# Optimization experiments

Measured on AMD Instinct MI355X. Metric: run time of the kernel, lower is better.

Reference implementation:

```python
import jax, jax.numpy as jnp
import numpy as np

COMMITMENT_COST = 0.25


def setup_inputs() -> dict:
    key = jax.random.key(0)
    k1, k2 = jax.random.split(key)
    inputs = jax.random.normal(k1, (16, 4096, 256), dtype=jnp.float32)
    codewords = jax.random.normal(k2, (1024, 256), dtype=jnp.float32)
    return {"inputs": inputs, "codewords": codewords}


def reference(inputs, codewords):
    # inputs: (*, D), codewords: (K, D)
    D = codewords.shape[-1]
    flat = inputs.reshape(-1, D)  # (N, D)
    x_sq = jnp.sum(flat * flat, axis=-1, keepdims=True)            # (N, 1)
    c_sq = jnp.sum(codewords * codewords, axis=-1)                 # (K,)
    distances = x_sq - 2.0 * (flat @ codewords.T) + c_sq           # (N, K)
    encoding_indices = jnp.argmin(distances, axis=1)               # (N,)
    quantized = codewords[encoding_indices].reshape(inputs.shape)  # (*, D)
    # Straight-through estimator
    quantized_st = inputs + jax.lax.stop_gradient(quantized - inputs)
    quantizing_loss = jnp.mean((quantized_st - jax.lax.stop_gradient(inputs)) ** 2)
    commitment_loss = jnp.mean((jax.lax.stop_gradient(quantized_st) - inputs) ** 2)
    loss = quantizing_loss + COMMITMENT_COST * commitment_loss
    return quantized_st, encoding_indices.reshape(inputs.shape[:-1]), loss
```

## Files before the change

kernel.cpp:

```cpp
#include <hip/hip_runtime.h>
#include <math.h>

typedef _Float16 v8h __attribute__((ext_vector_type(8)));
typedef float v4f __attribute__((ext_vector_type(4)));

constexpr int D      = 256;
constexpr int NTILE  = 64;
constexpr int KS     = 8;
constexpr int TILE_B = 8192;
constexpr int WIN_B  = 16384;
#define GUARD 2.0f

__global__ void vq_prep(const float* __restrict__ cw, unsigned short* __restrict__ img) {
    int gid = blockIdx.x * 256 + threadIdx.x;
    int t  = gid >> 9;
    int r  = gid & 511;
    int ks = r >> 6;
    int l  = r & 63;
    int cand = t * 16 + (l & 15);
    int k0   = ks * 32 + (l >> 4) * 8;
    const float* src = cw + (size_t)cand * D + k0;
    float4 t0 = *(const float4*)(src);
    float4 t1 = *(const float4*)(src + 4);
    v8h h;
    h[0] = (_Float16)t0.x; h[1] = (_Float16)t0.y;
    h[2] = (_Float16)t0.z; h[3] = (_Float16)t0.w;
    h[4] = (_Float16)t1.x; h[5] = (_Float16)t1.y;
    h[6] = (_Float16)t1.z; h[7] = (_Float16)t1.w;
    *(v8h*)((char*)img + (size_t)gid * 16) = h;
}

__global__ void vq_csq(const float* __restrict__ cw, float* __restrict__ csq) {
    int k = blockIdx.x * blockDim.x + threadIdx.x;
    const float4* p = reinterpret_cast<const float4*>(cw + (size_t)k * D);
    float s = 0.f;
    #pragma unroll 8
    for (int i = 0; i < D / 4; ++i) {
        float4 v = p[i];
        s += v.x * v.x; s += v.y * v.y; s += v.z * v.z; s += v.w * v.w;
    }
    csq[k] = s;
}

__launch_bounds__(256, 2)
__global__ void vq_mfma(const float* __restrict__ inp,
                        const unsigned short* __restrict__ img,
                        const float* __restrict__ csq,
                        int* __restrict__ pack,
                        float* __restrict__ xsqbuf) {
    __shared__ char smem[2][WIN_B];

    const int tid  = threadIdx.x;
    const int lane = tid & 63;
    const int w    = tid >> 6;
    const int lr   = lane & 15;
    const int q    = lane >> 4;
    const int base = blockIdx.x * 128 + w * 32;

    #pragma unroll
    for (int i = 0; i < 4; ++i) {
        int off = i * 4096 + w * 1024;
        __builtin_amdgcn_global_load_lds(
            (const __attribute__((address_space(1))) unsigned int*)((const char*)img + off + lane * 16),
            (__attribute__((address_space(3))) unsigned int*)(&smem[0][off]),
            16, 0, 0);
    }

    v8h a2[2][8];
    #pragma unroll
    for (int m = 0; m < 2; ++m) {
        const float* rp = inp + (size_t)(base + m * 16 + lr) * D + q * 8;
        float sq = 0.f;
        #pragma unroll
        for (int ks = 0; ks < KS; ++ks) {
            float4 t0 = *(const float4*)(rp + ks * 32);
            float4 t1 = *(const float4*)(rp + ks * 32 + 4);
            sq = fmaf(t0.x, t0.x, sq); sq = fmaf(t0.y, t0.y, sq);
            sq = fmaf(t0.z, t0.z, sq); sq = fmaf(t0.w, t0.w, sq);
            sq = fmaf(t1.x, t1.x, sq); sq = fmaf(t1.y, t1.y, sq);
            sq = fmaf(t1.z, t1.z, sq); sq = fmaf(t1.w, t1.w, sq);
            v8h h;
            h[0] = (_Float16)(-2.f * t0.x); h[1] = (_Float16)(-2.f * t0.y);
            h[2] = (_Float16)(-2.f * t0.z); h[3] = (_Float16)(-2.f * t0.w);
            h[4] = (_Float16)(-2.f * t1.x); h[5] = (_Float16)(-2.f * t1.y);
            h[6] = (_Float16)(-2.f * t1.z); h[7] = (_Float16)(-2.f * t1.w);
            a2[m][ks] = h;
        }
        sq += __shfl_xor(sq, 16);
        sq += __shfl_xor(sq, 32);
        if (q == 0) xsqbuf[base + m * 16 + lr] = sq;
    }

    const float BIGF = __uint_as_float(0x7F000000u);
    float v1[2][4], v2[2][4];
    #pragma unroll
    for (int m = 0; m < 2; ++m)
        #pragma unroll
        for (int r = 0; r < 4; ++r) { v1[m][r] = BIGF; v2[m][r] = BIGF; }

    asm volatile("s_waitcnt vmcnt(0)" ::: "memory");
    __builtin_amdgcn_s_barrier();
    __builtin_amdgcn_sched_barrier(0);

    int cur = 0;
    for (int win = 0; win < NTILE / 2; ++win) {
        if (win + 1 < NTILE / 2) {
            const char* srct = (const char*)img + (size_t)(win + 1) * WIN_B;
            #pragma unroll
            for (int i = 0; i < 4; ++i) {
                int off = i * 4096 + w * 1024;
                __builtin_amdgcn_global_load_lds(
                    (const __attribute__((address_space(1))) unsigned int*)(srct + off + lane * 16),
                    (__attribute__((address_space(3))) unsigned int*)(&smem[cur ^ 1][off]),
                    16, 0, 0);
            }
        }
        float cqA = csq[(2 * win) * 16 + lr] + 4096.f;
        float cqB = csq[(2 * win + 1) * 16 + lr] + 4096.f;

        const char* bb = smem[cur];
        v4f aA0 = {cqA, cqA, cqA, cqA}; v4f aA1 = aA0;
        v4f aB0 = {cqB, cqB, cqB, cqB}; v4f aB1 = aB0;
        #pragma unroll
        for (int ks = 0; ks < KS; ++ks) {
            v8h bA = *(const v8h*)(bb + ks * 1024 + lane * 16);
            v8h bB = *(const v8h*)(bb + TILE_B + ks * 1024 + lane * 16);
            aA0 = __builtin_amdgcn_mfma_f32_16x16x32_f16(a2[0][ks], bA, aA0, 0, 0, 0);
            aB0 = __builtin_amdgcn_mfma_f32_16x16x32_f16(a2[0][ks], bB, aB0, 0, 0, 0);
            aA1 = __builtin_amdgcn_mfma_f32_16x16x32_f16(a2[1][ks], bA, aA1, 0, 0, 0);
            aB1 = __builtin_amdgcn_mfma_f32_16x16x32_f16(a2[1][ks], bB, aB1, 0, 0, 0);
        }
        unsigned idxA = (unsigned)((2 * win) * 16) | (unsigned)lr;
        unsigned idxB = (unsigned)((2 * win + 1) * 16) | (unsigned)lr;
        #pragma unroll
        for (int r = 0; r < 4; ++r) {
            float f;
            f = __uint_as_float(((__float_as_uint(aA0[r]) + 0x200u) & 0xFFFFFC00u) | idxA);
            { float mx = fmaxf(v1[0][r], f); v2[0][r] = fminf(v2[0][r], mx); v1[0][r] = fminf(v1[0][r], f); }
            f = __uint_as_float(((__float_as_uint(aA1[r]) + 0x200u) & 0xFFFFFC00u) | idxA);
            { float mx = fmaxf(v1[1][r], f); v2[1][r] = fminf(v2[1][r], mx); v1[1][r] = fminf(v1[1][r], f); }
            f = __uint_as_float(((__float_as_uint(aB0[r]) + 0x200u) & 0xFFFFFC00u) | idxB);
            { float mx = fmaxf(v1[0][r], f); v2[0][r] = fminf(v2[0][r], mx); v1[0][r] = fminf(v1[0][r], f); }
            f = __uint_as_float(((__float_as_uint(aB1[r]) + 0x200u) & 0xFFFFFC00u) | idxB);
            { float mx = fmaxf(v1[1][r], f); v2[1][r] = fminf(v2[1][r], mx); v1[1][r] = fminf(v1[1][r], f); }
        }

        asm volatile("s_waitcnt vmcnt(0)" ::: "memory");
        __builtin_amdgcn_s_barrier();
        __builtin_amdgcn_sched_barrier(0);
        cur ^= 1;
    }

    #pragma unroll
    for (int m = 0; m < 2; ++m)
        #pragma unroll
        for (int r = 0; r < 4; ++r) {
            float L0 = v1[m][r], L1 = v2[m][r], L2 = BIGF, L3 = BIGF;
            #pragma unroll
            for (int off = 8; off; off >>= 1) {
                float P0 = __shfl_xor(L0, off, 16);
                float P1 = __shfl_xor(L1, off, 16);
                float P2 = __shfl_xor(L2, off, 16);
                float P3 = __shfl_xor(L3, off, 16);
                float M0 = fminf(L0, P3), M1 = fminf(L1, P2);
                float M2 = fminf(L2, P1), M3 = fminf(L3, P0);
                float a0 = fminf(M0, M2), c0 = fmaxf(M0, M2);
                float b0 = fminf(M1, M3), d0 = fmaxf(M1, M3);
                L0 = fminf(a0, b0); L1 = fmaxf(a0, b0);
                L2 = fminf(c0, d0); L3 = fmaxf(c0, d0);
            }
            if (lr == 0) {
                int row = base + m * 16 + q * 4 + r;
                ((int4*)pack)[row] = make_int4(
                    (int)__float_as_uint(L0), (int)__float_as_uint(L1),
                    (int)__float_as_uint(L2), (int)__float_as_uint(L3));
            }
        }
}

__launch_bounds__(256)
__global__ void vq_out(const float* __restrict__ inp,
                       const float* __restrict__ cw,
                       const float* __restrict__ csq,
                       const int* __restrict__ pack,
                       const float* __restrict__ xsqbuf,
                       float* __restrict__ outq,
                       float* __restrict__ outi,
                       float* __restrict__ bsum) {
    __shared__ float s_l[4];
    const int tid  = threadIdx.x;
    const int lane = tid & 63;
    const int wv   = tid >> 6;
    const int g    = blockIdx.x * 256 + tid;
    const int row  = g >> 2;
    const int c    = g & 3;

    int4 pk = ((const int4*)pack)[row];
    float s0 = __uint_as_float((unsigned)pk.x);
    float s1 = __uint_as_float((unsigned)pk.y);
    float xq = xsqbuf[row];

    int   bi;
    float bd;
    bool rescue = (s1 - s0) < GUARD;
    if (rescue) {
        int cd = ((c == 0) ? pk.x : (c == 1) ? pk.y : (c == 2) ? pk.z : pk.w) & 1023;
        const float4* xp = (const float4*)(inp + (size_t)row * D);
        const float4* cp = (const float4*)(cw + (size_t)cd * D);
        float dot = 0.f, xsq = 0.f;
        #pragma unroll 8
        for (int i = 0; i < D / 4; ++i) {
            float4 xv = xp[i];
            float4 cv = cp[i];
            xsq = fmaf(xv.x, xv.x, xsq);
            xsq = fmaf(xv.y, xv.y, xsq);
            xsq = fmaf(xv.z, xv.z, xsq);
            xsq = fmaf(xv.w, xv.w, xsq);
            dot = fmaf(xv.x, cv.x, dot);
            dot = fmaf(xv.y, cv.y, dot);
            dot = fmaf(xv.z, cv.z, dot);
            dot = fmaf(xv.w, cv.w, dot);
        }
        float m2 = dot + dot;
        float t  = xsq - m2;
        float e  = t + csq[cd];
        bd = e; bi = cd;
        #pragma unroll
        for (int off = 1; off <= 2; off <<= 1) {
            float ev = __shfl_xor(bd, off, 4);
            int   iv = __shfl_xor(bi, off, 4);
            bool  tk = (ev < bd) || (ev == bd && iv < bi);
            bd = tk ? ev : bd;
            bi = tk ? iv : bi;
        }
    } else {
        bi = pk.x & 1023;
        bd = (s0 - 4096.f) + xq;
    }

    if (c == 0) outi[row] = (float)bi;

    float lc = (c == 0) ? bd : 0.f;
    #pragma unroll
    for (int off = 32; off; off >>= 1) lc += __shfl_xor(lc, off);
    if (lane == 0) s_l[wv] = lc;
    __syncthreads();
    if (tid == 0) bsum[blockIdx.x] = s_l[0] + s_l[1] + s_l[2] + s_l[3];

    const int rowbase = blockIdx.x * 64 + wv * 16;
    #pragma unroll 4
    for (int rr = 0; rr < 16; ++rr) {
        int bw = __shfl(bi, rr * 4, 64);
        float4 cv = *(const float4*)(cw + (size_t)bw * D + lane * 4);
        *(float4*)(outq + (size_t)(rowbase + rr) * D + lane * 4) = cv;
    }
}

__global__ void vq_finalize(const float* __restrict__ bsum, float* __restrict__ out_loss,
                            int nb, float scale) {
    __shared__ float s[4];
    int tid = threadIdx.x;
    float v = 0.f;
    for (int i = tid; i < nb; i += 256) v += bsum[i];
    #pragma unroll
    for (int off = 32; off; off >>= 1) v += __shfl_down(v, off, 64);
    if ((tid & 63) == 0) s[tid >> 6] = v;
    __syncthreads();
    if (tid == 0) out_loss[0] = (s[0] + s[1] + s[2] + s[3]) * scale;
}

extern "C" void kernel_launch(void* const* d_in, const int* in_sizes, int n_in,
                              void* d_out, int out_size, void* d_ws, size_t ws_size,
                              hipStream_t stream) {
    const float* inp = (const float*)d_in[0];
    const float* cw  = (const float*)d_in[1];
    float* out = (float*)d_out;
    const int N = in_sizes[0] / D;
    const int K = in_sizes[1] / D;

    char* ws = (char*)d_ws;
    unsigned short* img = (unsigned short*)ws;
    float* csq    = (float*)(ws + (size_t)K * D * 2);
    float* bsum   = csq + K;
    int*   pack   = (int*)(bsum + 1024);
    float* xsqbuf = (float*)(pack + (size_t)N * 4);

    float* outq = out;
    float* outi = out + (size_t)N * D;
    float* outl = outi + N;

    vq_prep<<<dim3((K * 32) / 256), dim3(256), 0, stream>>>(cw, img);
    vq_csq<<<dim3(K / 256), dim3(256), 0, stream>>>(cw, csq);

    vq_mfma<<<dim3(N / 128), dim3(256), 0, stream>>>(inp, img, csq, pack, xsqbuf);
    vq_out<<<dim3(N / 64), dim3(256), 0, stream>>>(inp, cw, csq, pack, xsqbuf,
                                                   outq, outi, bsum);
    vq_finalize<<<dim3(1), dim3(256), 0, stream>>>(bsum, outl, N / 64,
                                                   1.25f / ((float)N * (float)D));
}
```

Measured before the change: 99.54 us.

## Split codebook search across two grid halves and merge top-4 lists in output kernel

```diff
diff --git a/kernel.cpp b/kernel.cpp
--- a/kernel.cpp
+++ b/kernel.cpp
@@ -9,6 +9,7 @@
 constexpr int KS     = 8;
 constexpr int TILE_B = 8192;
 constexpr int WIN_B  = 16384;
+constexpr int HWIN   = 16;
 #define GUARD 2.0f
 
 __global__ void vq_prep(const float* __restrict__ cw, unsigned short* __restrict__ img) {
@@ -42,7 +43,7 @@
     csq[k] = s;
 }
 
-__launch_bounds__(256, 2)
+__launch_bounds__(256, 4)
 __global__ void vq_mfma(const float* __restrict__ inp,
                         const unsigned short* __restrict__ img,
                         const float* __restrict__ csq,
@@ -55,13 +56,15 @@
     const int w    = tid >> 6;
     const int lr   = lane & 15;
     const int q    = lane >> 4;
+    const int hh   = blockIdx.y;
     const int base = blockIdx.x * 128 + w * 32;
+    const char* imgh = (const char*)img + (size_t)hh * 32 * TILE_B;
 
     #pragma unroll
     for (int i = 0; i < 4; ++i) {
         int off = i * 4096 + w * 1024;
         __builtin_amdgcn_global_load_lds(
-            (const __attribute__((address_space(1))) unsigned int*)((const char*)img + off + lane * 16),
+            (const __attribute__((address_space(1))) unsigned int*)(imgh + off + lane * 16),
             (__attribute__((address_space(3))) unsigned int*)(&smem[0][off]),
             16, 0, 0);
     }
@@ -88,7 +91,7 @@
         }
         sq += __shfl_xor(sq, 16);
         sq += __shfl_xor(sq, 32);
-        if (q == 0) xsqbuf[base + m * 16 + lr] = sq;
+        if (hh == 0 && q == 0) xsqbuf[base + m * 16 + lr] = sq;
     }
 
     const float BIGF = __uint_as_float(0x7F000000u);
@@ -103,9 +106,9 @@
     __builtin_amdgcn_sched_barrier(0);
 
     int cur = 0;
-    for (int win = 0; win < NTILE / 2; ++win) {
-        if (win + 1 < NTILE / 2) {
-            const char* srct = (const char*)img + (size_t)(win + 1) * WIN_B;
+    for (int win = 0; win < HWIN; ++win) {
+        if (win + 1 < HWIN) {
+            const char* srct = imgh + (size_t)(win + 1) * WIN_B;
             #pragma unroll
             for (int i = 0; i < 4; ++i) {
                 int off = i * 4096 + w * 1024;
@@ -115,8 +118,10 @@
                     16, 0, 0);
             }
         }
-        float cqA = csq[(2 * win) * 16 + lr] + 4096.f;
-        float cqB = csq[(2 * win + 1) * 16 + lr] + 4096.f;
+        const int tA = hh * 32 + 2 * win;
+        const int tB = tA + 1;
+        float cqA = csq[tA * 16 + lr] + 4096.f;
+        float cqB = csq[tB * 16 + lr] + 4096.f;
 
         const char* bb = smem[cur];
         v4f aA0 = {cqA, cqA, cqA, cqA}; v4f aA1 = aA0;
@@ -130,8 +135,8 @@
             aA1 = __builtin_amdgcn_mfma_f32_16x16x32_f16(a2[1][ks], bA, aA1, 0, 0, 0);
             aB1 = __builtin_amdgcn_mfma_f32_16x16x32_f16(a2[1][ks], bB, aB1, 0, 0, 0);
         }
-        unsigned idxA = (unsigned)((2 * win) * 16) | (unsigned)lr;
-        unsigned idxB = (unsigned)((2 * win + 1) * 16) | (unsigned)lr;
+        unsigned idxA = (unsigned)(tA * 16) | (unsigned)lr;
+        unsigned idxB = (unsigned)(tB * 16) | (unsigned)lr;
         #pragma unroll
         for (int r = 0; r < 4; ++r) {
             float f;
@@ -171,7 +176,7 @@
             }
             if (lr == 0) {
                 int row = base + m * 16 + q * 4 + r;
-                ((int4*)pack)[row] = make_int4(
+                ((int4*)pack)[(size_t)row * 2 + hh] = make_int4(
                     (int)__float_as_uint(L0), (int)__float_as_uint(L1),
                     (int)__float_as_uint(L2), (int)__float_as_uint(L3));
             }
@@ -195,16 +200,26 @@
     const int row  = g >> 2;
     const int c    = g & 3;
 
-    int4 pk = ((const int4*)pack)[row];
-    float s0 = __uint_as_float((unsigned)pk.x);
-    float s1 = __uint_as_float((unsigned)pk.y);
+    int4 pa = ((const int4*)pack)[(size_t)row * 2 + 0];
+    int4 pb = ((const int4*)pack)[(size_t)row * 2 + 1];
+    float a0 = __uint_as_float((unsigned)pa.x), a1 = __uint_as_float((unsigned)pa.y);
+    float a2 = __uint_as_float((unsigned)pa.z), a3 = __uint_as_float((unsigned)pa.w);
+    float b0 = __uint_as_float((unsigned)pb.x), b1 = __uint_as_float((unsigned)pb.y);
+    float b2 = __uint_as_float((unsigned)pb.z), b3 = __uint_as_float((unsigned)pb.w);
+    float M0 = fminf(a0, b3), M1 = fminf(a1, b2), M2 = fminf(a2, b1), M3 = fminf(a3, b0);
+    float t0 = fminf(M0, M2), t2 = fmaxf(M0, M2);
+    float t1 = fminf(M1, M3), t3 = fmaxf(M1, M3);
+    float L0 = fminf(t0, t1), L1 = fmaxf(t0, t1);
+    float L2 = fminf(t2, t3), L3 = fmaxf(t2, t3);
+
     float xq = xsqbuf[row];
 
     int   bi;
     float bd;
-    bool rescue = (s1 - s0) < GUARD;
+    bool rescue = (L1 - L0) < GUARD;
     if (rescue) {
-        int cd = ((c == 0) ? pk.x : (c == 1) ? pk.y : (c == 2) ? pk.z : pk.w) & 1023;
+        float Lc = (c == 0) ? L0 : (c == 1) ? L1 : (c == 2) ? L2 : L3;
+        int cd = (int)(__float_as_uint(Lc) & 1023u);
         const float4* xp = (const float4*)(inp + (size_t)row * D);
         const float4* cp = (const float4*)(cw + (size_t)cd * D);
         float dot = 0.f, xsq = 0.f;
@@ -234,8 +249,8 @@
             bi = tk ? iv : bi;
         }
     } else {
-        bi = pk.x & 1023;
-        bd = (s0 - 4096.f) + xq;
+        bi = (int)(__float_as_uint(L0) & 1023u);
+        bd = (L0 - 4096.f) + xq;
     }
 
     if (c == 0) outi[row] = (float)bi;
@@ -283,7 +298,7 @@
     float* csq    = (float*)(ws + (size_t)K * D * 2);
     float* bsum   = csq + K;
     int*   pack   = (int*)(bsum + 1024);
-    float* xsqbuf = (float*)(pack + (size_t)N * 4);
+    float* xsqbuf = (float*)(pack + (size_t)N * 8);
 
     float* outq = out;
     float* outi = out + (size_t)N * D;
@@ -292,7 +307,7 @@
     vq_prep<<<dim3((K * 32) / 256), dim3(256), 0, stream>>>(cw, img);
     vq_csq<<<dim3(K / 256), dim3(256), 0, stream>>>(cw, csq);
 
-    vq_mfma<<<dim3(N / 128), dim3(256), 0, stream>>>(inp, img, csq, pack, xsqbuf);
+    vq_mfma<<<dim3(N / 128, 2), dim3(256), 0, stream>>>(inp, img, csq, pack, xsqbuf);
     vq_out<<<dim3(N / 64), dim3(256), 0, stream>>>(inp, cw, csq, pack, xsqbuf,
                                                    outq, outi, bsum);
     vq_finalize<<<dim3(1), dim3(256), 0, stream>>>(bsum, outl, N / 64,
```

New measurement: 111.1 us. +11.6%, slower.

## Fuse rescue/output stage into MFMA kernel via shared-memory handoff

Applied to the files above, without the earlier changes.

```diff
diff --git a/kernel.cpp b/kernel.cpp
--- a/kernel.cpp
+++ b/kernel.cpp
@@ -43,12 +43,18 @@
 }
 
 __launch_bounds__(256, 2)
-__global__ void vq_mfma(const float* __restrict__ inp,
+__global__ void vq_main(const float* __restrict__ inp,
+                        const float* __restrict__ cw,
                         const unsigned short* __restrict__ img,
                         const float* __restrict__ csq,
-                        int* __restrict__ pack,
-                        float* __restrict__ xsqbuf) {
-    __shared__ char smem[2][WIN_B];
+                        float* __restrict__ outq,
+                        float* __restrict__ outi,
+                        float* __restrict__ bsum) {
+    __shared__ char  smem[2][WIN_B];
+    __shared__ int4  s_pack[128];
+    __shared__ float s_xsq[128];
+    __shared__ int   s_win[128];
+    __shared__ float s_l[4];
 
     const int tid  = threadIdx.x;
     const int lane = tid & 63;
@@ -88,7 +94,7 @@
         }
         sq += __shfl_xor(sq, 16);
         sq += __shfl_xor(sq, 32);
-        if (q == 0) xsqbuf[base + m * 16 + lr] = sq;
+        if (q == 0) s_xsq[w * 32 + m * 16 + lr] = sq;
     }
 
     const float BIGF = __uint_as_float(0x7F000000u);
@@ -170,90 +176,81 @@
                 L2 = fminf(c0, d0); L3 = fmaxf(c0, d0);
             }
             if (lr == 0) {
-                int row = base + m * 16 + q * 4 + r;
-                ((int4*)pack)[row] = make_int4(
+                int rloc = m * 16 + q * 4 + r;
+                s_pack[w * 32 + rloc] = make_int4(
                     (int)__float_as_uint(L0), (int)__float_as_uint(L1),
                     (int)__float_as_uint(L2), (int)__float_as_uint(L3));
             }
         }
-}
-
-__launch_bounds__(256)
-__global__ void vq_out(const float* __restrict__ inp,
-                       const float* __restrict__ cw,
-                       const float* __restrict__ csq,
-                       const int* __restrict__ pack,
-                       const float* __restrict__ xsqbuf,
-                       float* __restrict__ outq,
-                       float* __restrict__ outi,
-                       float* __restrict__ bsum) {
-    __shared__ float s_l[4];
-    const int tid  = threadIdx.x;
-    const int lane = tid & 63;
-    const int wv   = tid >> 6;
-    const int g    = blockIdx.x * 256 + tid;
-    const int row  = g >> 2;
-    const int c    = g & 3;
-
-    int4 pk = ((const int4*)pack)[row];
-    float s0 = __uint_as_float((unsigned)pk.x);
-    float s1 = __uint_as_float((unsigned)pk.y);
-    float xq = xsqbuf[row];
-
-    int   bi;
-    float bd;
-    bool rescue = (s1 - s0) < GUARD;
-    if (rescue) {
-        int cd = ((c == 0) ? pk.x : (c == 1) ? pk.y : (c == 2) ? pk.z : pk.w) & 1023;
-        const float4* xp = (const float4*)(inp + (size_t)row * D);
-        const float4* cp = (const float4*)(cw + (size_t)cd * D);
-        float dot = 0.f, xsq = 0.f;
-        #pragma unroll 8
-        for (int i = 0; i < D / 4; ++i) {
-            float4 xv = xp[i];
-            float4 cv = cp[i];
-            xsq = fmaf(xv.x, xv.x, xsq);
-            xsq = fmaf(xv.y, xv.y, xsq);
-            xsq = fmaf(xv.z, xv.z, xsq);
-            xsq = fmaf(xv.w, xv.w, xsq);
-            dot = fmaf(xv.x, cv.x, dot);
-            dot = fmaf(xv.y, cv.y, dot);
-            dot = fmaf(xv.z, cv.z, dot);
-            dot = fmaf(xv.w, cv.w, dot);
-        }
-        float m2 = dot + dot;
-        float t  = xsq - m2;
-        float e  = t + csq[cd];
-        bd = e; bi = cd;
-        #pragma unroll
-        for (int off = 1; off <= 2; off <<= 1) {
-            float ev = __shfl_xor(bd, off, 4);
-            int   iv = __shfl_xor(bi, off, 4);
-            bool  tk = (ev < bd) || (ev == bd && iv < bi);
-            bd = tk ? ev : bd;
-            bi = tk ? iv : bi;
-        }
-    } else {
-        bi = pk.x & 1023;
-        bd = (s0 - 4096.f) + xq;
-    }
-
-    if (c == 0) outi[row] = (float)bi;
-
-    float lc = (c == 0) ? bd : 0.f;
-    #pragma unroll
-    for (int off = 32; off; off >>= 1) lc += __shfl_xor(lc, off);
-    if (lane == 0) s_l[wv] = lc;
+
+    const int c = lane & 3;
+    float lacc = 0.f;
+    #pragma unroll
+    for (int h = 0; h < 2; ++h) {
+        int rloc = h * 16 + (lane >> 2);
+        int grow = base + rloc;
+        int4 pk = s_pack[w * 32 + rloc];
+        float L0 = __uint_as_float((unsigned)pk.x);
+        float L1 = __uint_as_float((unsigned)pk.y);
+        float L2 = __uint_as_float((unsigned)pk.z);
+        float L3 = __uint_as_float((unsigned)pk.w);
+        float xq = s_xsq[w * 32 + rloc];
+
+        int   bi;
+        float bd;
+        bool rescue = (L1 - L0) < GUARD;
+        if (rescue) {
+            float Lc = (c == 0) ? L0 : (c == 1) ? L1 : (c == 2) ? L2 : L3;
+            int cd = (int)(__float_as_uint(Lc) & 1023u);
+            const float4* xp = (const float4*)(inp + (size_t)grow * D);
+            const float4* cp = (const float4*)(cw + (size_t)cd * D);
+            float dot = 0.f, xsq = 0.f;
+            #pragma unroll 8
+            for (int i = 0; i < D / 4; ++i) {
+                float4 xv = xp[i];
+                float4 cv = cp[i];
+                xsq = fmaf(xv.x, xv.x, xsq);
+                xsq = fmaf(xv.y, xv.y, xsq);
+                xsq = fmaf(xv.z, xv.z, xsq);
+                xsq = fmaf(xv.w, xv.w, xsq);
+                dot = fmaf(xv.x, cv.x, dot);
+                dot = fmaf(xv.y, cv.y, dot);
+                dot = fmaf(xv.z, cv.z, dot);
+                dot = fmaf(xv.w, cv.w, dot);
+            }
+            float m2 = dot + dot;
+            float t  = xsq - m2;
+            float e  = t + csq[cd];
+            bd = e; bi = cd;
+            #pragma unroll
+            for (int off = 1; off <= 2; off <<= 1) {
+                float ev = __shfl_xor(bd, off, 4);
+                int   iv = __shfl_xor(bi, off, 4);
+                bool  tk = (ev < bd) || (ev == bd && iv < bi);
+                bd = tk ? ev : bd;
+                bi = tk ? iv : bi;
+            }
+        } else {
+            bi = (int)(__float_as_uint(L0) & 1023u);
+            bd = (L0 - 4096.f) + xq;
+        }
+
+        if (c == 0) { s_win[w * 32 + rloc] = bi; lacc += bd; }
+    }
+
+    #pragma unroll 4
+    for (int rr = 0; rr < 32; ++rr) {
+        int bw = s_win[w * 32 + rr];
+        float4 cv = *(const float4*)(cw + (size_t)bw * D + lane * 4);
+        *(float4*)(outq + (size_t)(base + rr) * D + lane * 4) = cv;
+        if (lane == 0) outi[base + rr] = (float)bw;
+    }
+
+    #pragma unroll
+    for (int off = 32; off; off >>= 1) lacc += __shfl_xor(lacc, off);
+    if (lane == 0) s_l[w] = lacc;
     __syncthreads();
     if (tid == 0) bsum[blockIdx.x] = s_l[0] + s_l[1] + s_l[2] + s_l[3];
-
-    const int rowbase = blockIdx.x * 64 + wv * 16;
-    #pragma unroll 4
-    for (int rr = 0; rr < 16; ++rr) {
-        int bw = __shfl(bi, rr * 4, 64);
-        float4 cv = *(const float4*)(cw + (size_t)bw * D + lane * 4);
-        *(float4*)(outq + (size_t)(rowbase + rr) * D + lane * 4) = cv;
-    }
 }
 
 __global__ void vq_finalize(const float* __restrict__ bsum, float* __restrict__ out_loss,
@@ -280,10 +277,8 @@
 
     char* ws = (char*)d_ws;
     unsigned short* img = (unsigned short*)ws;
-    float* csq    = (float*)(ws + (size_t)K * D * 2);
-    float* bsum   = csq + K;
-    int*   pack   = (int*)(bsum + 1024);
-    float* xsqbuf = (float*)(pack + (size_t)N * 4);
+    float* csq  = (float*)(ws + (size_t)K * D * 2);
+    float* bsum = csq + K;
 
     float* outq = out;
     float* outi = out + (size_t)N * D;
@@ -292,9 +287,8 @@
     vq_prep<<<dim3((K * 32) / 256), dim3(256), 0, stream>>>(cw, img);
     vq_csq<<<dim3(K / 256), dim3(256), 0, stream>>>(cw, csq);
 
-    vq_mfma<<<dim3(N / 128), dim3(256), 0, stream>>>(inp, img, csq, pack, xsqbuf);
-    vq_out<<<dim3(N / 64), dim3(256), 0, stream>>>(inp, cw, csq, pack, xsqbuf,
-                                                   outq, outi, bsum);
-    vq_finalize<<<dim3(1), dim3(256), 0, stream>>>(bsum, outl, N / 64,
+    vq_main<<<dim3(N / 128), dim3(256), 0, stream>>>(inp, cw, img, csq,
+                                                     outq, outi, bsum);
+    vq_finalize<<<dim3(1), dim3(256), 0, stream>>>(bsum, outl, N / 128,
                                                    1.25f / ((float)N * (float)D));
 }
```

Result: faster. 96.58 us (-3.0%).
